# Performance work log

Hardware: AMD Instinct MI355X
Metric: run time of the kernel (lower is better)

Reference implementation:

```python
import jax, jax.numpy as jnp
import numpy as np

V = 0.1


def _swap_np():
    d = 2
    s = np.zeros((d * d, d * d))
    for i in range(d):
        for j in range(d):
            s[i * d + j, j * d + i] = 1.0
    k, I = np.kron, np.eye
    s0123 = k(I(d ** 2), s)
    s01234 = k(s0123, I(d))
    s0123456 = k(s01234, s)
    s01234567 = k(s0123456, I(d))
    s0123456789 = k(s01234567, s)
    s012345678911 = k(s0123456789, I(d ** 2))
    s01 = k(s, I(d ** 10))
    s12 = k(k(I(d), s), I(d ** 9))
    s23 = k(k(I(d ** 2), s), I(d ** 8))
    s34 = k(k(I(d ** 3), s), I(d ** 7))
    s45 = k(k(I(d ** 4), s), I(d ** 6))
    s56 = k(k(I(d ** 5), s), I(d ** 5))
    s67 = k(k(I(d ** 6), s), I(d ** 4))
    s78 = k(k(I(d ** 7), s), I(d ** 3))
    s89 = k(k(I(d ** 8), s), I(d ** 2))
    s90 = k(k(I(d ** 9), s), I(d))
    s11 = k(I(d ** 10), s)
    chain = [s01, s12, s23, s34, s45, s56, s67, s78, s89, s90, s11,
             s90, s89, s78, s67, s56, s45, s34, s23, s12, s01]
    swap_far = chain[0]
    for mat in chain[1:]:
        swap_far = swap_far @ mat
    return swap_far @ s012345678911


def _obj_np():
    p = np.zeros((4, 4, 4, 4))
    for q in range(4):
        for w in range(4):
            for e in range(4):
                for r in range(4):
                    if q != w and w != e and e != r and q != r:
                        if q == e or w == r:
                            if q == e and w == r:
                                p[q, w, e, r] = (1 - V) / 2 ** 8
                            else:
                                p[q, w, e, r] = (3 + 5 * V) / (2 ** 8 * 3)
                        else:
                            p[q, w, e, r] = (3 + 13 * V) / (2 ** 8 * 3)
                    else:
                        p[q, w, e, r] = (1 - V) / 2 ** 8
    return p


SWAP = jnp.asarray(_swap_np(), dtype=jnp.float32)   # [4096, 4096] permutation
OBJ = jnp.asarray(_obj_np(), dtype=jnp.float32)     # [4, 4, 4, 4] target distribution
TRIU_R, TRIU_C = np.triu_indices(8, k=1)            # 28 strictly-upper entries, row-major


def setup_inputs() -> dict:
    key = jax.random.key(0)
    # small init keeps POVM element M4 = I - M1 - M2 - M3 near-PSD so the KL log is finite
    params = 0.1 * jax.random.normal(key, (121,), dtype=jnp.float32)
    return {"params": params}


def _generate_state(a):
    a = jnp.exp(a)
    a = a / jnp.linalg.norm(a)                       # F.normalize(dim=0)
    psi = jnp.concatenate([a[0:1], jnp.zeros(3, a.dtype), a[1:5]])  # [8]
    # 4-fold tensor product -> [4096]
    return jnp.kron(jnp.kron(jnp.kron(psi, psi), psi), psi)


def _generate_povm(x):
    eigen = jax.nn.softmax(x[:32].reshape(4, 8), axis=0)  # eigenvalues sum to 1 per column
    offd = x[32:116].reshape(3, 28)

    def make(e, od):
        A = jnp.zeros((8, 8), x.dtype).at[TRIU_R, TRIU_C].set(od)
        A = A - A.T                                  # antisymmetric generator
        U = jax.scipy.linalg.expm(A)                 # orthogonal
        return (U * e[None, :]) @ U.T                # U diag(e) U^T

    m012 = jax.vmap(make)(eigen[:3], offd)           # [3, 8, 8]
    m3 = jnp.eye(8, dtype=x.dtype) - m012.sum(axis=0)
    return jnp.concatenate([m012, m3[None]], axis=0)  # [4, 8, 8]


def reference(params):
    state = _generate_state(params[0:5])             # [4096]
    state = SWAP @ state
    rou = jnp.outer(state, state)                    # [4096, 4096] density matrix
    m = _generate_povm(params[5:121])                # [4, 8, 8]
    # trace(rou @ (Mq (x) Mw (x) Me (x) Mr)) via per-leg contraction instead of
    # 256 dense 4096x4096 matmuls: rou[I,J] * Ma[J,I] with I=(i,j,k,l), J=(m,n,o,p)
    R = rou.reshape((8,) * 8)
    result = jnp.einsum('ijklmnop,qmi,wnj,eok,rpl->qwer', R, m, m, m, m)  # [4,4,4,4]
    y = jnp.sum(OBJ * jnp.log(OBJ / result))         # KL divergence
    return y, result, m
```

## Files before the change

kernel.cpp:

```cpp
#include <hip/hip_runtime.h>
#include <math.h>

#define NT 256


__global__ __launch_bounds__(NT) void qu4_all(const float* __restrict__ P,
                                              float* __restrict__ out)
{
    const int tid  = threadIdx.x;
    const int wave = tid >> 6;
    const int lane = tid & 63;

    __shared__ __align__(16) float Ucol[240];
    __shared__ __align__(16) float Esh[32];
    __shared__ __align__(16) float psiF[8];
    __shared__ __align__(16) float Mf[256];
    __shared__ __align__(16) float Tc2[3072];
    __shared__ __align__(16) float Gs[21056];
    __shared__ __align__(16) float Hs[5184];
    __shared__ __align__(16) float HTs[5184];
    __shared__ float redC[16];

    if (wave == 0 && lane < 24) {
        const int a = lane >> 3, c = lane & 7;
        const float* Pb = P + 37 + a * 28;
        float B[8][8];
        #pragma unroll
        for (int r = 0; r < 8; r++) {
            B[r][r] = 0.f;
            #pragma unroll
            for (int u = r + 1; u < 8; u++) {
                float v = Pb[7*r - (r*(r-1))/2 + u - r - 1];
                B[r][u] = v;  B[u][r] = -v;
            }
        }
        float e[8], col[8];
        #pragma unroll
        for (int u = 0; u < 8; u++) { e[u] = (u == c) ? 1.f : 0.f; col[u] = e[u]; }
        #pragma unroll
        for (int k = 9; k >= 1; --k) {
            float nc[8];
            #pragma unroll
            for (int r = 0; r < 8; r++) {
                float s0 = B[r][0]*col[0] + B[r][1]*col[1];
                float s1 = B[r][2]*col[2] + B[r][3]*col[3];
                float s2 = B[r][4]*col[4] + B[r][5]*col[5];
                float s3 = B[r][6]*col[6] + B[r][7]*col[7];
                nc[r] = (s0 + s1) + (s2 + s3);
            }
            const float ik = 1.f / (float)k;
            #pragma unroll
            for (int r = 0; r < 8; r++) col[r] = e[r] + nc[r] * ik;
        }
        float* uc = &Ucol[a*80 + c*8];
        *(float4*)&uc[0] = make_float4(col[0], col[1], col[2], col[3]);
        *(float4*)&uc[4] = make_float4(col[4], col[5], col[6], col[7]);
    } else if (wave == 1) {
        if (lane < 8) {
            float x0 = P[5 + lane], x1 = P[13 + lane], x2 = P[21 + lane], x3 = P[29 + lane];
            float mx = fmaxf(fmaxf(x0, x1), fmaxf(x2, x3));
            float e0 = expf(x0-mx), e1 = expf(x1-mx), e2 = expf(x2-mx), e3 = expf(x3-mx);
            float s = e0 + e1 + e2 + e3;
            Esh[lane] = e0/s; Esh[8+lane] = e1/s; Esh[16+lane] = e2/s; Esh[24+lane] = e3/s;
        } else if (lane == 8) {
            float av[5]; float ss = 0.f;
            #pragma unroll
            for (int i = 0; i < 5; i++) { av[i] = expf(P[i]); ss += av[i]*av[i]; }
            float inv = 1.f / sqrtf(ss);
            psiF[0] = av[0]*inv; psiF[1] = 0.f; psiF[2] = 0.f; psiF[3] = 0.f;
            psiF[4] = av[1]*inv; psiF[5] = av[2]*inv; psiF[6] = av[3]*inv; psiF[7] = av[4]*inv;
        }
    }
    __syncthreads();

    {
        const int a = wave, r = lane >> 3, c = lane & 7;
        float m;
        if (a < 3) {
            float4 e0 = *(const float4*)&Esh[a*8], e1 = *(const float4*)&Esh[a*8+4];
            float ev[8] = {e0.x,e0.y,e0.z,e0.w, e1.x,e1.y,e1.z,e1.w};
            float s = 0.f;
            #pragma unroll
            for (int u = 0; u < 8; u++)
                s += Ucol[a*80 + u*8 + r] * ev[u] * Ucol[a*80 + u*8 + c];
            m = s;
        } else {
            float s = 0.f;
            #pragma unroll
            for (int a2 = 0; a2 < 3; a2++) {
                float4 e0 = *(const float4*)&Esh[a2*8], e1 = *(const float4*)&Esh[a2*8+4];
                float ev[8] = {e0.x,e0.y,e0.z,e0.w, e1.x,e1.y,e1.z,e1.w};
                #pragma unroll
                for (int u = 0; u < 8; u++)
                    s += Ucol[a2*80 + u*8 + r] * ev[u] * Ucol[a2*80 + u*8 + c];
            }
            m = ((r == c) ? 1.f : 0.f) - s;
        }
        Mf[a*64 + lane] = m;
        out[257 + a*64 + lane] = m;
    }

    {
        const int a = wave, m = lane >> 3, j = lane & 7;
        const int j0 = j >> 2, j1 = (j >> 1) & 1;
        float4 m0 = *(const float4*)&Mf[a*64 + m*8], m1 = *(const float4*)&Mf[a*64 + m*8 + 4];
        float mav[8] = {m0.x,m0.y,m0.z,m0.w, m1.x,m1.y,m1.z,m1.w};
        float4 q0 = *(const float4*)&psiF[0], q1 = *(const float4*)&psiF[4];
        float ps[8] = {q0.x,q0.y,q0.z,q0.w, q1.x,q1.y,q1.z,q1.w};
        float pA[4], pB[4];
        #pragma unroll
        for (int c1 = 0; c1 < 2; c1++)
            #pragma unroll
            for (int i1 = 0; i1 < 2; i1++)
                pA[c1*2+i1] = j0 ? ps[c1*4+i1*2+1] : ps[c1*4+i1*2];
        #pragma unroll
        for (int i2 = 0; i2 < 2; i2++)
            #pragma unroll
            for (int c2 = 0; c2 < 2; c2++)
                pB[i2*2+c2] = j1 ? ps[i2*4+2+c2] : ps[i2*4+c2];
        #pragma unroll
        for (int h = 0; h < 8; h++) {
            const int c1 = h >> 2, c2 = (h >> 1) & 1, r4 = h & 1;
            float v = 0.f;
            #pragma unroll
            for (int i1 = 0; i1 < 2; i1++)
                #pragma unroll
                for (int i2 = 0; i2 < 2; i2++)
                    v += mav[r4*4 + i1*2 + i2] * pA[c1*2+i1] * pB[i2*2+c2];
            Tc2[h*384 + a*96 + m*12 + j] = v;
        }
    }
    __syncthreads();

    {
        const int p = tid >> 4, m = (tid >> 1) & 7, nh = tid & 1;
        const int a = p >> 2, b = p & 3;
        float Tv[8][8];
        #pragma unroll
        for (int h = 0; h < 8; h++) {
            float4 t0 = *(const float4*)&Tc2[h*384 + a*96 + m*12];
            float4 t1 = *(const float4*)&Tc2[h*384 + a*96 + m*12 + 4];
            Tv[h][0]=t0.x; Tv[h][1]=t0.y; Tv[h][2]=t0.z; Tv[h][3]=t0.w;
            Tv[h][4]=t1.x; Tv[h][5]=t1.y; Tv[h][6]=t1.z; Tv[h][7]=t1.w;
        }
        float mb[4][8];
        #pragma unroll
        for (int n4 = 0; n4 < 4; n4++) {
            float4 v0 = *(const float4*)&Mf[b*64 + (nh*4 + n4)*8];
            float4 v1 = *(const float4*)&Mf[b*64 + (nh*4 + n4)*8 + 4];
            mb[n4][0]=v0.x; mb[n4][1]=v0.y; mb[n4][2]=v0.z; mb[n4][3]=v0.w;
            mb[n4][4]=v1.x; mb[n4][5]=v1.y; mb[n4][6]=v1.z; mb[n4][7]=v1.w;
        }
        #pragma unroll
        for (int n4 = 0; n4 < 4; n4++) {
            const int n = nh*4 + n4;
            float acc[16];
            #pragma unroll
            for (int t = 0; t < 16; t++) {
                const int h  = (t>>3)*4 + ((t>>2)&1)*2 + (t&1);
                const int r3 = (t>>1)&1;
                acc[t] = mb[n4][r3]   * Tv[h][r3]
                       + mb[n4][2+r3] * Tv[h][2+r3]
                       + mb[n4][4+r3] * Tv[h][4+r3]
                       + mb[n4][6+r3] * Tv[h][6+r3];
            }
            float* gp = &Gs[p*1316 + m*164 + n*20];
            *(float4*)&gp[0]  = make_float4(acc[0],  acc[1],  acc[2],  acc[3]);
            *(float4*)&gp[4]  = make_float4(acc[4],  acc[5],  acc[6],  acc[7]);
            *(float4*)&gp[8]  = make_float4(acc[8],  acc[9],  acc[10], acc[11]);
            *(float4*)&gp[12] = make_float4(acc[12], acc[13], acc[14], acc[15]);
        }
    }
    __syncthreads();

    {
        const int p = tid >> 4, g = (tid >> 1) & 7, hh = tid & 1;
        const int c1 = g >> 2, c2 = (g >> 1) & 1, r3 = g & 1;
        float4 q0 = *(const float4*)&psiF[0], q1 = *(const float4*)&psiF[4];
        float ps[8] = {q0.x,q0.y,q0.z,q0.w, q1.x,q1.y,q1.z,q1.w};
        float pr[4];
        #pragma unroll
        for (int xx = 0; xx < 4; xx++) pr[xx] = r3 ? ps[4+xx] : ps[xx];
        float acc0[8], acc1[8];
        #pragma unroll
        for (int t = 0; t < 8; t++) { acc0[t] = 0.f; acc1[t] = 0.f; }
        #pragma unroll
        for (int m1 = 0; m1 < 2; m1++)
        #pragma unroll
        for (int m2 = 0; m2 < 2; m2++)
        #pragma unroll
        for (int n0 = 0; n0 < 2; n0++)
        #pragma unroll
        for (int n1 = 0; n1 < 2; n1++) {
            const int m = c2*4 + m1*2 + m2;
            const int n = n0*4 + n1*2 + c1;
            const float* gp = &Gs[p*1316 + m*164 + n*20 + hh*8];
            float4 g0 = *(const float4*)&gp[0], g1 = *(const float4*)&gp[4];
            const float w1 = pr[m1*2 + n0];
            const float wa = w1 * ps[m2*4 + n1*2];
            const float wb = w1 * ps[m2*4 + n1*2 + 1];
            float gv[8] = {g0.x,g0.y,g0.z,g0.w, g1.x,g1.y,g1.z,g1.w};
            #pragma unroll
            for (int t = 0; t < 8; t++) { acc0[t] += wa*gv[t]; acc1[t] += wb*gv[t]; }
        }
        {
            const int tV0 = c1*8 + c2*4 + r3*2;
            float* hb0 = &Hs[p*324 + tV0*20 + hh*8];
            *(float4*)&hb0[0] = make_float4(acc0[0], acc0[1], acc0[2], acc0[3]);
            *(float4*)&hb0[4] = make_float4(acc0[4], acc0[5], acc0[6], acc0[7]);
            float* hb1 = &Hs[p*324 + (tV0+1)*20 + hh*8];
            *(float4*)&hb1[0] = make_float4(acc1[0], acc1[1], acc1[2], acc1[3]);
            *(float4*)&hb1[4] = make_float4(acc1[4], acc1[5], acc1[6], acc1[7]);
            #pragma unroll
            for (int t = 0; t < 8; t++) {
                HTs[p*324 + (hh*8 + t)*20 + tV0]     = acc0[t];
                HTs[p*324 + (hh*8 + t)*20 + tV0 + 1] = acc1[t];
            }
        }
    }
    __syncthreads();

    {
        const int tile = tid >> 4, tv = tid & 15;
        const int tp = tile >> 2, tq = tile & 3;
        float4 hp[4][4];
        #pragma unroll
        for (int i = 0; i < 4; i++) {
            const float* hb = &Hs[(tp*4 + i)*324 + tv*20];
            hp[i][0] = *(const float4*)&hb[0];  hp[i][1] = *(const float4*)&hb[4];
            hp[i][2] = *(const float4*)&hb[8];  hp[i][3] = *(const float4*)&hb[12];
        }
        float acc[4][4];
        #pragma unroll
        for (int jq = 0; jq < 4; jq++) {
            const float* tb = &HTs[(tq*4 + jq)*324 + tv*20];
            float4 h0 = *(const float4*)&tb[0],  h1 = *(const float4*)&tb[4];
            float4 h2 = *(const float4*)&tb[8],  h3 = *(const float4*)&tb[12];
            #pragma unroll
            for (int i = 0; i < 4; i++) {
                acc[i][jq] = hp[i][0].x*h0.x + hp[i][0].y*h0.y + hp[i][0].z*h0.z + hp[i][0].w*h0.w
                           + hp[i][1].x*h1.x + hp[i][1].y*h1.y + hp[i][1].z*h1.z + hp[i][1].w*h1.w
                           + hp[i][2].x*h2.x + hp[i][2].y*h2.y + hp[i][2].z*h2.z + hp[i][2].w*h2.w
                           + hp[i][3].x*h3.x + hp[i][3].y*h3.y + hp[i][3].z*h3.z + hp[i][3].w*h3.w;
            }
        }
        #pragma unroll
        for (int i = 0; i < 4; i++)
            #pragma unroll
            for (int j = 0; j < 4; j++) {
                float v = acc[i][j];
                v += __shfl_xor(v, 1, 64);
                v += __shfl_xor(v, 2, 64);
                v += __shfl_xor(v, 4, 64);
                v += __shfl_xor(v, 8, 64);
                acc[i][j] = v;
            }
        const int li = tv >> 2, lj = tv & 3;
        float Cv = 0.f;
        #pragma unroll
        for (int i = 0; i < 4; i++)
            #pragma unroll
            for (int j = 0; j < 4; j++)
                if (li == i && lj == j) Cv = acc[i][j];
        const int idx = (tp*4 + li)*16 + (tq*4 + lj);
        out[1 + idx] = Cv;
        const int q = (idx>>6)&3, w = (idx>>4)&3, e = (idx>>2)&3, rr = idx&3;
        const float OA = 0.9f/256.f, OB = 3.5f/768.f, OC = 4.3f/768.f;
        float obj;
        if (q != w && w != e && e != rr && q != rr)
            obj = (q == e || w == rr) ? ((q == e && w == rr) ? OA : OB) : OC;
        else obj = OA;
        float klt = obj * logf(obj / Cv);
        klt += __shfl_xor(klt, 1, 64);
        klt += __shfl_xor(klt, 2, 64);
        klt += __shfl_xor(klt, 4, 64);
        klt += __shfl_xor(klt, 8, 64);
        if (tv == 0) redC[tile] = klt;
    }
    __syncthreads();
    if (tid == 0) {
        float s = 0.f;
        #pragma unroll
        for (int i = 0; i < 16; i++) s += redC[i];
        out[0] = s;
    }
}

extern "C" void kernel_launch(void* const* d_in, const int* in_sizes, int n_in,
                              void* d_out, int out_size, void* d_ws, size_t ws_size,
                              hipStream_t stream)
{
    const float* P = (const float*)d_in[0];
    float* out = (float*)d_out;
    qu4_all<<<1, NT, 0, stream>>>(P, out);
}
```

Baseline: 13.38 us.

## Store U rows for vectorized POVM build, use recursive-halving shuffle reduction

Computes U^T rows instead of columns (negated generator) and stores them padded, so each POVM entry reads two float4 rows rather than strided scalars. The 16 per-thread partial sums are combined with a recursive-halving transpose shuffle (15 shuffles instead of 64), and the transposed H writes become float2 stores. The final 16-way sum moves to a wave shuffle. Together these cut LDS traffic and shuffle count in a tiny single-block kernel, at the cost of more complex select logic.

```diff
diff --git a/kernel.cpp b/kernel.cpp
--- a/kernel.cpp
+++ b/kernel.cpp
@@ -11,7 +11,7 @@
     const int wave = tid >> 6;
     const int lane = tid & 63;
 
-    __shared__ __align__(16) float Ucol[240];
+    __shared__ __align__(16) float Urow[288];
     __shared__ __align__(16) float Esh[32];
     __shared__ __align__(16) float psiF[8];
     __shared__ __align__(16) float Mf[256];
@@ -22,39 +22,39 @@
     __shared__ float redC[16];
 
     if (wave == 0 && lane < 24) {
-        const int a = lane >> 3, c = lane & 7;
+        const int a = lane >> 3, r = lane & 7;
         const float* Pb = P + 37 + a * 28;
-        float B[8][8];
-        #pragma unroll
-        for (int r = 0; r < 8; r++) {
-            B[r][r] = 0.f;
-            #pragma unroll
-            for (int u = r + 1; u < 8; u++) {
-                float v = Pb[7*r - (r*(r-1))/2 + u - r - 1];
-                B[r][u] = v;  B[u][r] = -v;
+        float Bn[8][8];
+        #pragma unroll
+        for (int x = 0; x < 8; x++) {
+            Bn[x][x] = 0.f;
+            #pragma unroll
+            for (int u = x + 1; u < 8; u++) {
+                float v = Pb[7*x - (x*(x-1))/2 + u - x - 1];
+                Bn[x][u] = -v;  Bn[u][x] = v;
             }
         }
         float e[8], col[8];
         #pragma unroll
-        for (int u = 0; u < 8; u++) { e[u] = (u == c) ? 1.f : 0.f; col[u] = e[u]; }
+        for (int u = 0; u < 8; u++) { e[u] = (u == r) ? 1.f : 0.f; col[u] = e[u]; }
         #pragma unroll
         for (int k = 9; k >= 1; --k) {
             float nc[8];
             #pragma unroll
-            for (int r = 0; r < 8; r++) {
-                float s0 = B[r][0]*col[0] + B[r][1]*col[1];
-                float s1 = B[r][2]*col[2] + B[r][3]*col[3];
-                float s2 = B[r][4]*col[4] + B[r][5]*col[5];
-                float s3 = B[r][6]*col[6] + B[r][7]*col[7];
-                nc[r] = (s0 + s1) + (s2 + s3);
+            for (int x = 0; x < 8; x++) {
+                float s0 = Bn[x][0]*col[0] + Bn[x][1]*col[1];
+                float s1 = Bn[x][2]*col[2] + Bn[x][3]*col[3];
+                float s2 = Bn[x][4]*col[4] + Bn[x][5]*col[5];
+                float s3 = Bn[x][6]*col[6] + Bn[x][7]*col[7];
+                nc[x] = (s0 + s1) + (s2 + s3);
             }
             const float ik = 1.f / (float)k;
             #pragma unroll
-            for (int r = 0; r < 8; r++) col[r] = e[r] + nc[r] * ik;
-        }
-        float* uc = &Ucol[a*80 + c*8];
-        *(float4*)&uc[0] = make_float4(col[0], col[1], col[2], col[3]);
-        *(float4*)&uc[4] = make_float4(col[4], col[5], col[6], col[7]);
+            for (int x = 0; x < 8; x++) col[x] = e[x] + nc[x] * ik;
+        }
+        float* ur = &Urow[a*96 + r*12];
+        *(float4*)&ur[0] = make_float4(col[0], col[1], col[2], col[3]);
+        *(float4*)&ur[4] = make_float4(col[4], col[5], col[6], col[7]);
     } else if (wave == 1) {
         if (lane < 8) {
             float x0 = P[5 + lane], x1 = P[13 + lane], x2 = P[21 + lane], x3 = P[29 + lane];
@@ -77,22 +77,20 @@
         const int a = wave, r = lane >> 3, c = lane & 7;
         float m;
         if (a < 3) {
-            float4 e0 = *(const float4*)&Esh[a*8], e1 = *(const float4*)&Esh[a*8+4];
-            float ev[8] = {e0.x,e0.y,e0.z,e0.w, e1.x,e1.y,e1.z,e1.w};
-            float s = 0.f;
-            #pragma unroll
-            for (int u = 0; u < 8; u++)
-                s += Ucol[a*80 + u*8 + r] * ev[u] * Ucol[a*80 + u*8 + c];
-            m = s;
+            float4 r0 = *(const float4*)&Urow[a*96 + r*12], r1 = *(const float4*)&Urow[a*96 + r*12 + 4];
+            float4 c0 = *(const float4*)&Urow[a*96 + c*12], c1 = *(const float4*)&Urow[a*96 + c*12 + 4];
+            float4 e0 = *(const float4*)&Esh[a*8],          e1 = *(const float4*)&Esh[a*8 + 4];
+            m = r0.x*e0.x*c0.x + r0.y*e0.y*c0.y + r0.z*e0.z*c0.z + r0.w*e0.w*c0.w
+              + r1.x*e1.x*c1.x + r1.y*e1.y*c1.y + r1.z*e1.z*c1.z + r1.w*e1.w*c1.w;
         } else {
             float s = 0.f;
             #pragma unroll
             for (int a2 = 0; a2 < 3; a2++) {
-                float4 e0 = *(const float4*)&Esh[a2*8], e1 = *(const float4*)&Esh[a2*8+4];
-                float ev[8] = {e0.x,e0.y,e0.z,e0.w, e1.x,e1.y,e1.z,e1.w};
-                #pragma unroll
-                for (int u = 0; u < 8; u++)
-                    s += Ucol[a2*80 + u*8 + r] * ev[u] * Ucol[a2*80 + u*8 + c];
+                float4 r0 = *(const float4*)&Urow[a2*96 + r*12], r1 = *(const float4*)&Urow[a2*96 + r*12 + 4];
+                float4 c0 = *(const float4*)&Urow[a2*96 + c*12], c1 = *(const float4*)&Urow[a2*96 + c*12 + 4];
+                float4 e0 = *(const float4*)&Esh[a2*8],          e1 = *(const float4*)&Esh[a2*8 + 4];
+                s += r0.x*e0.x*c0.x + r0.y*e0.y*c0.y + r0.z*e0.z*c0.z + r0.w*e0.w*c0.w
+                   + r1.x*e1.x*c1.x + r1.y*e1.y*c1.y + r1.z*e1.z*c1.z + r1.w*e1.w*c1.w;
             }
             m = ((r == c) ? 1.f : 0.f) - s;
         }
@@ -212,10 +210,8 @@
             *(float4*)&hb1[0] = make_float4(acc1[0], acc1[1], acc1[2], acc1[3]);
             *(float4*)&hb1[4] = make_float4(acc1[4], acc1[5], acc1[6], acc1[7]);
             #pragma unroll
-            for (int t = 0; t < 8; t++) {
-                HTs[p*324 + (hh*8 + t)*20 + tV0]     = acc0[t];
-                HTs[p*324 + (hh*8 + t)*20 + tV0 + 1] = acc1[t];
-            }
+            for (int t = 0; t < 8; t++)
+                *(float2*)&HTs[p*324 + (hh*8 + t)*20 + tV0] = make_float2(acc0[t], acc1[t]);
         }
     }
     __syncthreads();
@@ -230,7 +226,7 @@
             hp[i][0] = *(const float4*)&hb[0];  hp[i][1] = *(const float4*)&hb[4];
             hp[i][2] = *(const float4*)&hb[8];  hp[i][3] = *(const float4*)&hb[12];
         }
-        float acc[4][4];
+        float acc[16];
         #pragma unroll
         for (int jq = 0; jq < 4; jq++) {
             const float* tb = &HTs[(tq*4 + jq)*324 + tv*20];
@@ -238,30 +234,42 @@
             float4 h2 = *(const float4*)&tb[8],  h3 = *(const float4*)&tb[12];
             #pragma unroll
             for (int i = 0; i < 4; i++) {
-                acc[i][jq] = hp[i][0].x*h0.x + hp[i][0].y*h0.y + hp[i][0].z*h0.z + hp[i][0].w*h0.w
-                           + hp[i][1].x*h1.x + hp[i][1].y*h1.y + hp[i][1].z*h1.z + hp[i][1].w*h1.w
-                           + hp[i][2].x*h2.x + hp[i][2].y*h2.y + hp[i][2].z*h2.z + hp[i][2].w*h2.w
-                           + hp[i][3].x*h3.x + hp[i][3].y*h3.y + hp[i][3].z*h3.z + hp[i][3].w*h3.w;
-            }
-        }
-        #pragma unroll
-        for (int i = 0; i < 4; i++)
-            #pragma unroll
-            for (int j = 0; j < 4; j++) {
-                float v = acc[i][j];
-                v += __shfl_xor(v, 1, 64);
-                v += __shfl_xor(v, 2, 64);
-                v += __shfl_xor(v, 4, 64);
-                v += __shfl_xor(v, 8, 64);
-                acc[i][j] = v;
-            }
+                acc[i*4+jq] = hp[i][0].x*h0.x + hp[i][0].y*h0.y + hp[i][0].z*h0.z + hp[i][0].w*h0.w
+                            + hp[i][1].x*h1.x + hp[i][1].y*h1.y + hp[i][1].z*h1.z + hp[i][1].w*h1.w
+                            + hp[i][2].x*h2.x + hp[i][2].y*h2.y + hp[i][2].z*h2.z + hp[i][2].w*h2.w
+                            + hp[i][3].x*h3.x + hp[i][3].y*h3.y + hp[i][3].z*h3.z + hp[i][3].w*h3.w;
+            }
+        }
+        const bool s1 = (tv & 1) != 0;
+        float a8[8];
+        #pragma unroll
+        for (int k = 0; k < 8; k++) {
+            float xk = s1 ? acc[2*k+1] : acc[2*k];
+            float yk = s1 ? acc[2*k]   : acc[2*k+1];
+            a8[k] = xk + __shfl_xor(yk, 1, 64);
+        }
+        const bool s2 = (tv & 2) != 0;
+        float a4[4];
+        #pragma unroll
+        for (int k = 0; k < 4; k++) {
+            float xk = s2 ? a8[2*k+1] : a8[2*k];
+            float yk = s2 ? a8[2*k]   : a8[2*k+1];
+            a4[k] = xk + __shfl_xor(yk, 2, 64);
+        }
+        const bool s4 = (tv & 4) != 0;
+        float a2[2];
+        #pragma unroll
+        for (int k = 0; k < 2; k++) {
+            float xk = s4 ? a4[2*k+1] : a4[2*k];
+            float yk = s4 ? a4[2*k]   : a4[2*k+1];
+            a2[k] = xk + __shfl_xor(yk, 4, 64);
+        }
+        const bool s8 = (tv & 8) != 0;
+        float xk = s8 ? a2[1] : a2[0];
+        float yk = s8 ? a2[0] : a2[1];
+        const float Cv = xk + __shfl_xor(yk, 8, 64);
+
         const int li = tv >> 2, lj = tv & 3;
-        float Cv = 0.f;
-        #pragma unroll
-        for (int i = 0; i < 4; i++)
-            #pragma unroll
-            for (int j = 0; j < 4; j++)
-                if (li == i && lj == j) Cv = acc[i][j];
         const int idx = (tp*4 + li)*16 + (tq*4 + lj);
         out[1 + idx] = Cv;
         const int q = (idx>>6)&3, w = (idx>>4)&3, e = (idx>>2)&3, rr = idx&3;
@@ -278,11 +286,13 @@
         if (tv == 0) redC[tile] = klt;
     }
     __syncthreads();
-    if (tid == 0) {
-        float s = 0.f;
-        #pragma unroll
-        for (int i = 0; i < 16; i++) s += redC[i];
-        out[0] = s;
+    if (wave == 0 && lane < 16) {
+        float v = redC[lane];
+        v += __shfl_xor(v, 1, 64);
+        v += __shfl_xor(v, 2, 64);
+        v += __shfl_xor(v, 4, 64);
+        v += __shfl_xor(v, 8, 64);
+        if (lane == 0) out[0] = v;
     }
 }
 
```

Result: faster. 13.10 us (-2.1%).
